# Optimization experiments

Hardware: AMD Instinct MI355X
Metric: run time of the kernel (lower is better)

## Reference

```python
import jax, jax.numpy as jnp
import numpy as np

HIDDEN = 256

def setup_inputs() -> dict:
    key = jax.random.key(0)
    k1, k2, k3, k4 = jax.random.split(key, 4)
    B, S, H = 64, 4096, HIDDEN
    o_all_time = jax.random.normal(k1, (B, S, H), dtype=jnp.float32)
    scale = 1.0 / np.sqrt(H)
    W_t = jax.random.uniform(k2, (H, H), dtype=jnp.float32, minval=-scale, maxval=scale)
    W_F = jax.random.uniform(k3, (H, H), dtype=jnp.float32, minval=-scale, maxval=scale)
    v_F = jax.random.uniform(k4, (H, 1), dtype=jnp.float32, minval=-scale, maxval=scale)
    return {"o_all_time": o_all_time, "W_t": W_t, "W_F": W_F, "v_F": v_F}

def reference(o_all_time, W_t, W_F, v_F):
    # o_all_time: (B, S, H)
    o_last = o_all_time[:, -1, :]                       # (B, H)
    # time attention: scores = o_last @ (o_all_time @ W_t)^T over seq
    M_t = jnp.einsum('bsh,hk->bsk', o_all_time, W_t)    # (B, S, H)
    scores_time = jnp.einsum('bh,bsh->bs', o_last, M_t) # (B, S)
    alpha_t = jax.nn.softmax(scores_time, axis=-1)      # (B, S)
    output_T = jnp.einsum('bs,bsh->bh', alpha_t, o_all_time)  # (B, H)
    # feature attention: softmax over seq of v_F^T tanh(W_F x)
    M_f = jnp.tanh(jnp.einsum('bsh,hk->bsk', o_all_time, W_F))  # (B, S, H)
    scores_feature = jnp.einsum('bsh,hk->bsk', M_f, v_F)[..., 0]  # (B, S)
    alpha_f = jax.nn.softmax(scores_feature, axis=1)    # (B, S)
    output_F = jnp.einsum('bs,bsh->bh', alpha_f, o_all_time)  # (B, H)
    return jnp.concatenate([output_T, output_F], axis=1)  # (B, 2H)
```

## Files before the change

kernel.cpp:

```cpp
#include <hip/hip_runtime.h>
#include <hip/hip_bf16.h>
#include <stdint.h>

#define HID 256
#define BATCH 64
#define SEQ 4096

typedef __attribute__((ext_vector_type(8))) short bf16x8;
typedef __attribute__((ext_vector_type(4))) short short4v;
typedef __attribute__((ext_vector_type(4))) float f32x4;

static __device__ __forceinline__ unsigned short f2bf(float f) {
    union { float f; uint32_t u; } v; v.f = f;
    uint32_t u = v.u;
    return (unsigned short)((u + 0x7FFF + ((u >> 16) & 1)) >> 16);
}

static __device__ __forceinline__ float fast_tanh(float x) {
    float cx = fminf(fmaxf(x, -15.f), 15.f);
    float e = __expf(2.f * cx);
    return (e - 1.f) / (e + 1.f);
}

__global__ __launch_bounds__(256) void prep_wft(const float* __restrict__ WF,
                                                unsigned short* __restrict__ WFt) {
    int c = blockIdx.x, h = threadIdx.x;
    WFt[c * HID + h] = f2bf(WF[h * HID + c]);
}

__global__ __launch_bounds__(256) void prep_ut(const float* __restrict__ o,
                                               const float* __restrict__ Wt,
                                               float* __restrict__ ut) {
    __shared__ float ol[HID];
    int b = blockIdx.x, h = threadIdx.x;
    ol[h] = o[(size_t)(b * SEQ + SEQ - 1) * HID + h];
    __syncthreads();
    const float* wrow = Wt + h * HID;
    float acc = 0.f;
    #pragma unroll 8
    for (int k = 0; k < HID; k++) acc += wrow[k] * ol[k];
    ut[b * HID + h] = acc;
}

__global__ __launch_bounds__(256, 4) void scores_kernel(const float* __restrict__ o,
                                                        const unsigned short* __restrict__ WFt,
                                                        const float* __restrict__ ut,
                                                        const float* __restrict__ vF,
                                                        float* __restrict__ stOut,
                                                        float* __restrict__ sfOut) {
    __shared__ unsigned short o_sm[64 * HID];
    __shared__ float u_sm[HID];
    __shared__ float red_sm[64 * 4];
    __shared__ float sfr[4 * 64];

    int t = threadIdx.x;
    int lane = t & 63, w = t >> 6;
    int bid = blockIdx.x;
    int b = bid >> 6;
    int s0 = (bid & 63) << 6;
    int lm = lane & 15, lg = lane >> 4;

    u_sm[t] = ut[b * HID + t];
    __syncthreads();

    const float* pbase = o + (size_t)(b * SEQ + s0) * HID + t * 4;
    const float4 u4 = *(const float4*)&u_sm[lane << 2];

    float4 va[8], vb[8];
    #pragma unroll
    for (int j = 0; j < 8; j++) va[j] = *(const float4*)(pbase + j * 1024);
    #pragma unroll
    for (int j = 0; j < 8; j++) vb[j] = *(const float4*)(pbase + (j + 8) * 1024);

    #pragma unroll
    for (int j = 0; j < 16; j++) {
        float4 v = (j < 8) ? va[j & 7] : vb[j & 7];
        int row = j * 4 + w;
        float p = v.x * u4.x + v.y * u4.y + v.z * u4.z + v.w * u4.w;
        p += __shfl_xor(p, 1);
        p += __shfl_xor(p, 2);
        p += __shfl_xor(p, 4);
        p += __shfl_xor(p, 8);
        if (lm == 0) red_sm[(row << 2) + lg] = p;
        int byte = (row << 9) + (lane << 3);
        byte ^= (row & 7) << 4;
        short4v sv;
        sv.x = (short)f2bf(v.x); sv.y = (short)f2bf(v.y);
        sv.z = (short)f2bf(v.z); sv.w = (short)f2bf(v.w);
        *(short4v*)((char*)o_sm + byte) = sv;
    }
    __syncthreads();

    if (t < 64) {
        const float* r4 = &red_sm[t << 2];
        stOut[(size_t)b * SEQ + s0 + t] = r4[0] + r4[1] + r4[2] + r4[3];
    }

    f32x4 acc[4][4];
    #pragma unroll
    for (int ar = 0; ar < 4; ar++)
        #pragma unroll
        for (int cb = 0; cb < 4; cb++)
            acc[ar][cb] = (f32x4){0.f, 0.f, 0.f, 0.f};

    int cw = w << 6;

    #pragma unroll
    for (int kk = 0; kk < 8; kk++) {
        int h0 = kk * 32 + lg * 8;
        bf16x8 bf[4], af[4];
        #pragma unroll
        for (int cb = 0; cb < 4; cb++) {
            int c = cw + cb * 16 + lm;
            bf[cb] = *(const bf16x8*)(WFt + (size_t)c * HID + h0);
        }
        #pragma unroll
        for (int ar = 0; ar < 4; ar++) {
            int row = ar * 16 + lm;
            int byte = (row << 9) + h0 * 2;
            byte ^= (row & 7) << 4;
            af[ar] = *(const bf16x8*)((const char*)o_sm + byte);
        }
        #pragma unroll
        for (int ar = 0; ar < 4; ar++)
            #pragma unroll
            for (int cb = 0; cb < 4; cb++)
                acc[ar][cb] = __builtin_amdgcn_mfma_f32_16x16x32_bf16(af[ar], bf[cb], acc[ar][cb], 0, 0, 0);
    }

    float vf[4];
    #pragma unroll
    for (int cb = 0; cb < 4; cb++) vf[cb] = vF[cw + cb * 16 + lm];

    #pragma unroll
    for (int ar = 0; ar < 4; ar++) {
        #pragma unroll
        for (int i = 0; i < 4; i++) {
            float p = 0.f;
            #pragma unroll
            for (int cb = 0; cb < 4; cb++)
                p += fast_tanh(acc[ar][cb][i]) * vf[cb];
            p += __shfl_xor(p, 1);
            p += __shfl_xor(p, 2);
            p += __shfl_xor(p, 4);
            p += __shfl_xor(p, 8);
            if (lm == 0) sfr[w * 64 + ar * 16 + lg * 4 + i] = p;
        }
    }
    __syncthreads();
    if (t < 64) {
        float s = sfr[t] + sfr[64 + t] + sfr[128 + t] + sfr[192 + t];
        sfOut[(size_t)b * SEQ + s0 + t] = s;
    }
}

template <bool MAXOP>
static __device__ __forceinline__ float block_reduce(float v, float* sh) {
    #pragma unroll
    for (int m = 1; m < 64; m <<= 1) {
        float o = __shfl_xor(v, m);
        v = MAXOP ? fmaxf(v, o) : (v + o);
    }
    int w = threadIdx.x >> 6;
    if ((threadIdx.x & 63) == 0) sh[w] = v;
    __syncthreads();
    float r = MAXOP ? fmaxf(fmaxf(sh[0], sh[1]), fmaxf(sh[2], sh[3]))
                    : (sh[0] + sh[1] + sh[2] + sh[3]);
    __syncthreads();
    return r;
}

__global__ __launch_bounds__(256) void stats_kernel(const float* __restrict__ st,
                                                    const float* __restrict__ sf,
                                                    float* __restrict__ stats) {
    __shared__ float sh[4];
    int b = blockIdx.x, t = threadIdx.x;
    const float* pt = st + (size_t)b * SEQ;
    const float* pf = sf + (size_t)b * SEQ;
    float vt[16], vf[16], mT = -1e30f, mF = -1e30f;
    #pragma unroll
    for (int j = 0; j < 16; j++) {
        vt[j] = pt[t + j * 256]; mT = fmaxf(mT, vt[j]);
        vf[j] = pf[t + j * 256]; mF = fmaxf(mF, vf[j]);
    }
    mT = block_reduce<true>(mT, sh);
    mF = block_reduce<true>(mF, sh);
    float sT = 0.f, sF = 0.f;
    #pragma unroll
    for (int j = 0; j < 16; j++) {
        sT += __expf(vt[j] - mT);
        sF += __expf(vf[j] - mF);
    }
    sT = block_reduce<false>(sT, sh);
    sF = block_reduce<false>(sF, sh);
    if (t == 0) {
        stats[b * 4 + 0] = mT;
        stats[b * 4 + 1] = sT;
        stats[b * 4 + 2] = mF;
        stats[b * 4 + 3] = sF;
    }
}

__global__ __launch_bounds__(256, 4) void out_kernel(const float* __restrict__ o,
                                                     const float* __restrict__ st,
                                                     const float* __restrict__ sf,
                                                     const float* __restrict__ stats,
                                                     float* __restrict__ out) {
    __shared__ float wT[128], wF[128];
    __shared__ float4 redT[4][64], redF[4][64];
    int bid = blockIdx.x;
    int b = bid >> 5, chunk = bid & 31, s0 = chunk << 7;
    int t = threadIdx.x;

    if (t < 128) {
        float mT = stats[b * 4 + 0], isT = 1.f / stats[b * 4 + 1];
        float mF = stats[b * 4 + 2], isF = 1.f / stats[b * 4 + 3];
        wT[t] = __expf(st[(size_t)b * SEQ + s0 + t] - mT) * isT;
        wF[t] = __expf(sf[(size_t)b * SEQ + s0 + t] - mF) * isF;
    }
    __syncthreads();

    int hc = t & 63, sl = t >> 6;
    const float* ob = o + (size_t)(b * SEQ + s0) * HID + hc * 4;
    float4 aT = {0.f, 0.f, 0.f, 0.f}, aF = {0.f, 0.f, 0.f, 0.f};
    #pragma unroll
    for (int ii = 0; ii < 4; ii++) {
        float4 v[8];
        #pragma unroll
        for (int k = 0; k < 8; k++) {
            int r = sl + (ii * 8 + k) * 4;
            v[k] = *(const float4*)(ob + (size_t)r * HID);
        }
        #pragma unroll
        for (int k = 0; k < 8; k++) {
            int r = sl + (ii * 8 + k) * 4;
            float wt = wT[r], wf = wF[r];
            aT.x += wt * v[k].x; aT.y += wt * v[k].y; aT.z += wt * v[k].z; aT.w += wt * v[k].w;
            aF.x += wf * v[k].x; aF.y += wf * v[k].y; aF.z += wf * v[k].z; aF.w += wf * v[k].w;
        }
    }
    redT[sl][hc] = aT;
    redF[sl][hc] = aF;
    __syncthreads();

    int hcc = t >> 2, i = t & 3;
    float sumT = 0.f, sumF = 0.f;
    #pragma unroll
    for (int p = 0; p < 4; p++) {
        sumT += ((const float*)&redT[p][hcc])[i];
        sumF += ((const float*)&redF[p][hcc])[i];
    }
    atomicAdd(out + (size_t)b * 512 + t, sumT);
    atomicAdd(out + (size_t)b * 512 + 256 + t, sumF);
}

extern "C" void kernel_launch(void* const* d_in, const int* in_sizes, int n_in,
                              void* d_out, int out_size, void* d_ws, size_t ws_size,
                              hipStream_t stream) {
    const float* o  = (const float*)d_in[0];
    const float* Wt = (const float*)d_in[1];
    const float* WF = (const float*)d_in[2];
    const float* vF = (const float*)d_in[3];
    float* out = (float*)d_out;
    char* ws = (char*)d_ws;

    unsigned short* WFt = (unsigned short*)ws;
    float* ut    = (float*)(ws + 131072);
    float* stS   = (float*)(ws + 196608);
    float* sfS   = (float*)(ws + 196608 + 1048576);
    float* stats = (float*)(ws + 196608 + 2097152);

    hipMemsetAsync(d_out, 0, (size_t)BATCH * 512 * sizeof(float), stream);
    prep_wft<<<256, 256, 0, stream>>>(WF, WFt);
    prep_ut<<<BATCH, 256, 0, stream>>>(o, Wt, ut);
    scores_kernel<<<BATCH * 64, 256, 0, stream>>>(o, WFt, ut, vF, stS, sfS);
    stats_kernel<<<BATCH, 256, 0, stream>>>(stS, sfS, stats);
    out_kernel<<<BATCH * 32, 256, 0, stream>>>(o, stS, sfS, stats, out);
}
```

Before: 460.8 us.

## Fuse score, local softmax and weighted sum into one pass with combine

Computes per-tile softmax statistics and weighted partial sums inside the scores kernel using the bf16 tile already staged in shared memory. A small combine kernel then merges the partials with log-sum-exp rescaling. This removes the second full read of o, the stats kernel, the memset and the atomics, and merges the two prep kernels into one launch. In exchange, the weighted sums now use bf16-rounded inputs, which lowers accuracy.

```diff
diff --git a/kernel.cpp b/kernel.cpp
--- a/kernel.cpp
+++ b/kernel.cpp
@@ -16,42 +16,54 @@
     return (unsigned short)((u + 0x7FFF + ((u >> 16) & 1)) >> 16);
 }
 
+static __device__ __forceinline__ float bf2f(unsigned short b) {
+    union { uint32_t u; float f; } v; v.u = ((uint32_t)b) << 16;
+    return v.f;
+}
+
 static __device__ __forceinline__ float fast_tanh(float x) {
     float cx = fminf(fmaxf(x, -15.f), 15.f);
     float e = __expf(2.f * cx);
     return (e - 1.f) / (e + 1.f);
 }
 
-__global__ __launch_bounds__(256) void prep_wft(const float* __restrict__ WF,
-                                                unsigned short* __restrict__ WFt) {
-    int c = blockIdx.x, h = threadIdx.x;
-    WFt[c * HID + h] = f2bf(WF[h * HID + c]);
-}
-
-__global__ __launch_bounds__(256) void prep_ut(const float* __restrict__ o,
-                                               const float* __restrict__ Wt,
-                                               float* __restrict__ ut) {
+__global__ __launch_bounds__(256) void prep_kernel(const float* __restrict__ WF,
+                                                   const float* __restrict__ Wt,
+                                                   const float* __restrict__ o,
+                                                   unsigned short* __restrict__ WFt,
+                                                   float* __restrict__ ut) {
     __shared__ float ol[HID];
-    int b = blockIdx.x, h = threadIdx.x;
-    ol[h] = o[(size_t)(b * SEQ + SEQ - 1) * HID + h];
-    __syncthreads();
-    const float* wrow = Wt + h * HID;
-    float acc = 0.f;
-    #pragma unroll 8
-    for (int k = 0; k < HID; k++) acc += wrow[k] * ol[k];
-    ut[b * HID + h] = acc;
-}
-
-__global__ __launch_bounds__(256, 4) void scores_kernel(const float* __restrict__ o,
-                                                        const unsigned short* __restrict__ WFt,
-                                                        const float* __restrict__ ut,
-                                                        const float* __restrict__ vF,
-                                                        float* __restrict__ stOut,
-                                                        float* __restrict__ sfOut) {
-    __shared__ unsigned short o_sm[64 * HID];
+    int bid = blockIdx.x, t = threadIdx.x;
+    if (bid < 256) {
+        WFt[bid * HID + t] = f2bf(WF[t * HID + bid]);
+    } else {
+        int b = bid - 256;
+        ol[t] = o[(size_t)(b * SEQ + SEQ - 1) * HID + t];
+        __syncthreads();
+        const float* wrow = Wt + t * HID;
+        float acc = 0.f;
+        #pragma unroll 16
+        for (int k = 0; k < HID; k += 4) {
+            float4 w4 = *(const float4*)(wrow + k);
+            float4 o4 = *(const float4*)(ol + k);
+            acc += w4.x * o4.x + w4.y * o4.y + w4.z * o4.z + w4.w * o4.w;
+        }
+        ut[b * HID + t] = acc;
+    }
+}
+
+__global__ __launch_bounds__(256, 4) void fused_kernel(const float* __restrict__ o,
+                                                       const unsigned short* __restrict__ WFt,
+                                                       const float* __restrict__ ut,
+                                                       const float* __restrict__ vF,
+                                                       float* __restrict__ pT,
+                                                       float* __restrict__ pF,
+                                                       float* __restrict__ stats4) {
+    __shared__ __align__(16) unsigned short o_sm[64 * HID];
     __shared__ float u_sm[HID];
-    __shared__ float red_sm[64 * 4];
-    __shared__ float sfr[4 * 64];
+    __shared__ float red_sm[256];
+    __shared__ float sfr[256];
+    __shared__ float st_sm[64], sf_sm[64], wT_sm[64], wF_sm[64];
 
     int t = threadIdx.x;
     int lane = t & 63, w = t >> 6;
@@ -93,7 +105,7 @@
 
     if (t < 64) {
         const float* r4 = &red_sm[t << 2];
-        stOut[(size_t)b * SEQ + s0 + t] = r4[0] + r4[1] + r4[2] + r4[3];
+        st_sm[t] = r4[0] + r4[1] + r4[2] + r4[3];
     }
 
     f32x4 acc[4][4];
@@ -104,7 +116,6 @@
             acc[ar][cb] = (f32x4){0.f, 0.f, 0.f, 0.f};
 
     int cw = w << 6;
-
     #pragma unroll
     for (int kk = 0; kk < 8; kk++) {
         int h0 = kk * 32 + lg * 8;
@@ -148,110 +159,112 @@
         }
     }
     __syncthreads();
-    if (t < 64) {
-        float s = sfr[t] + sfr[64 + t] + sfr[128 + t] + sfr[192 + t];
-        sfOut[(size_t)b * SEQ + s0 + t] = s;
-    }
-}
-
-template <bool MAXOP>
-static __device__ __forceinline__ float block_reduce(float v, float* sh) {
-    #pragma unroll
-    for (int m = 1; m < 64; m <<= 1) {
-        float o = __shfl_xor(v, m);
-        v = MAXOP ? fmaxf(v, o) : (v + o);
-    }
-    int w = threadIdx.x >> 6;
-    if ((threadIdx.x & 63) == 0) sh[w] = v;
-    __syncthreads();
-    float r = MAXOP ? fmaxf(fmaxf(sh[0], sh[1]), fmaxf(sh[2], sh[3]))
-                    : (sh[0] + sh[1] + sh[2] + sh[3]);
-    __syncthreads();
-    return r;
-}
-
-__global__ __launch_bounds__(256) void stats_kernel(const float* __restrict__ st,
-                                                    const float* __restrict__ sf,
-                                                    float* __restrict__ stats) {
-    __shared__ float sh[4];
+    if (t < 64) sf_sm[t] = sfr[t] + sfr[64 + t] + sfr[128 + t] + sfr[192 + t];
+    __syncthreads();
+
+    if (t < 64) {
+        float vT = st_sm[t], vfv = sf_sm[t];
+        float mT = vT, mF = vfv;
+        #pragma unroll
+        for (int d = 1; d < 64; d <<= 1) {
+            mT = fmaxf(mT, __shfl_xor(mT, d));
+            mF = fmaxf(mF, __shfl_xor(mF, d));
+        }
+        float wT = __expf(vT - mT), wF = __expf(vfv - mF);
+        wT_sm[t] = wT; wF_sm[t] = wF;
+        float lT = wT, lF = wF;
+        #pragma unroll
+        for (int d = 1; d < 64; d <<= 1) {
+            lT += __shfl_xor(lT, d);
+            lF += __shfl_xor(lF, d);
+        }
+        if (t == 0) {
+            float* s4 = stats4 + (size_t)bid * 4;
+            s4[0] = mT; s4[1] = lT; s4[2] = mF; s4[3] = lF;
+        }
+    }
+    __syncthreads();
+
+    float4 aT = {0.f, 0.f, 0.f, 0.f}, aF = {0.f, 0.f, 0.f, 0.f};
+    #pragma unroll
+    for (int j = 0; j < 16; j++) {
+        int row = j * 4 + w;
+        int byte = (row << 9) + (lane << 3);
+        byte ^= (row & 7) << 4;
+        short4v sv = *(const short4v*)((const char*)o_sm + byte);
+        float x0 = bf2f((unsigned short)sv.x), x1 = bf2f((unsigned short)sv.y);
+        float x2 = bf2f((unsigned short)sv.z), x3 = bf2f((unsigned short)sv.w);
+        float wt = wT_sm[row], wf = wF_sm[row];
+        aT.x += wt * x0; aT.y += wt * x1; aT.z += wt * x2; aT.w += wt * x3;
+        aF.x += wf * x0; aF.y += wf * x1; aF.z += wf * x2; aF.w += wf * x3;
+    }
+    __syncthreads();
+    float4* pTa = (float4*)&o_sm[0];
+    float4* pFa = (float4*)&o_sm[2048];
+    pTa[w * 64 + lane] = aT;
+    pFa[w * 64 + lane] = aF;
+    __syncthreads();
+
+    if (t < 64) {
+        float4 s = pTa[t];
+        #pragma unroll
+        for (int ww = 1; ww < 4; ww++) {
+            float4 q = pTa[ww * 64 + t];
+            s.x += q.x; s.y += q.y; s.z += q.z; s.w += q.w;
+        }
+        *(float4*)(pT + (size_t)bid * HID + (t << 2)) = s;
+    } else if (t < 128) {
+        int tt = t - 64;
+        float4 s = pFa[tt];
+        #pragma unroll
+        for (int ww = 1; ww < 4; ww++) {
+            float4 q = pFa[ww * 64 + tt];
+            s.x += q.x; s.y += q.y; s.z += q.z; s.w += q.w;
+        }
+        *(float4*)(pF + (size_t)bid * HID + (tt << 2)) = s;
+    }
+}
+
+__global__ __launch_bounds__(256) void combine_kernel(const float* __restrict__ pT,
+                                                      const float* __restrict__ pF,
+                                                      const float* __restrict__ stats4,
+                                                      float* __restrict__ out) {
+    __shared__ float sMT[64], sLT[64], sMF[64], sLF[64], eT[64], eF[64];
+    __shared__ float sc[2];
     int b = blockIdx.x, t = threadIdx.x;
-    const float* pt = st + (size_t)b * SEQ;
-    const float* pf = sf + (size_t)b * SEQ;
-    float vt[16], vf[16], mT = -1e30f, mF = -1e30f;
-    #pragma unroll
-    for (int j = 0; j < 16; j++) {
-        vt[j] = pt[t + j * 256]; mT = fmaxf(mT, vt[j]);
-        vf[j] = pf[t + j * 256]; mF = fmaxf(mF, vf[j]);
-    }
-    mT = block_reduce<true>(mT, sh);
-    mF = block_reduce<true>(mF, sh);
-    float sT = 0.f, sF = 0.f;
-    #pragma unroll
-    for (int j = 0; j < 16; j++) {
-        sT += __expf(vt[j] - mT);
-        sF += __expf(vf[j] - mF);
-    }
-    sT = block_reduce<false>(sT, sh);
-    sF = block_reduce<false>(sF, sh);
-    if (t == 0) {
-        stats[b * 4 + 0] = mT;
-        stats[b * 4 + 1] = sT;
-        stats[b * 4 + 2] = mF;
-        stats[b * 4 + 3] = sF;
-    }
-}
-
-__global__ __launch_bounds__(256, 4) void out_kernel(const float* __restrict__ o,
-                                                     const float* __restrict__ st,
-                                                     const float* __restrict__ sf,
-                                                     const float* __restrict__ stats,
-                                                     float* __restrict__ out) {
-    __shared__ float wT[128], wF[128];
-    __shared__ float4 redT[4][64], redF[4][64];
-    int bid = blockIdx.x;
-    int b = bid >> 5, chunk = bid & 31, s0 = chunk << 7;
-    int t = threadIdx.x;
-
-    if (t < 128) {
-        float mT = stats[b * 4 + 0], isT = 1.f / stats[b * 4 + 1];
-        float mF = stats[b * 4 + 2], isF = 1.f / stats[b * 4 + 3];
-        wT[t] = __expf(st[(size_t)b * SEQ + s0 + t] - mT) * isT;
-        wF[t] = __expf(sf[(size_t)b * SEQ + s0 + t] - mF) * isF;
-    }
-    __syncthreads();
-
-    int hc = t & 63, sl = t >> 6;
-    const float* ob = o + (size_t)(b * SEQ + s0) * HID + hc * 4;
-    float4 aT = {0.f, 0.f, 0.f, 0.f}, aF = {0.f, 0.f, 0.f, 0.f};
-    #pragma unroll
-    for (int ii = 0; ii < 4; ii++) {
-        float4 v[8];
-        #pragma unroll
-        for (int k = 0; k < 8; k++) {
-            int r = sl + (ii * 8 + k) * 4;
-            v[k] = *(const float4*)(ob + (size_t)r * HID);
-        }
-        #pragma unroll
-        for (int k = 0; k < 8; k++) {
-            int r = sl + (ii * 8 + k) * 4;
-            float wt = wT[r], wf = wF[r];
-            aT.x += wt * v[k].x; aT.y += wt * v[k].y; aT.z += wt * v[k].z; aT.w += wt * v[k].w;
-            aF.x += wf * v[k].x; aF.y += wf * v[k].y; aF.z += wf * v[k].z; aF.w += wf * v[k].w;
-        }
-    }
-    redT[sl][hc] = aT;
-    redF[sl][hc] = aF;
-    __syncthreads();
-
-    int hcc = t >> 2, i = t & 3;
-    float sumT = 0.f, sumF = 0.f;
-    #pragma unroll
-    for (int p = 0; p < 4; p++) {
-        sumT += ((const float*)&redT[p][hcc])[i];
-        sumF += ((const float*)&redF[p][hcc])[i];
-    }
-    atomicAdd(out + (size_t)b * 512 + t, sumT);
-    atomicAdd(out + (size_t)b * 512 + 256 + t, sumF);
+    if (t < 64) {
+        const float* s4 = stats4 + (size_t)(b * 64 + t) * 4;
+        sMT[t] = s4[0]; sLT[t] = s4[1]; sMF[t] = s4[2]; sLF[t] = s4[3];
+    }
+    __syncthreads();
+    if (t < 64) {
+        float mT = sMT[t], mF = sMF[t];
+        #pragma unroll
+        for (int d = 1; d < 64; d <<= 1) {
+            mT = fmaxf(mT, __shfl_xor(mT, d));
+            mF = fmaxf(mF, __shfl_xor(mF, d));
+        }
+        float wT = __expf(sMT[t] - mT), wF = __expf(sMF[t] - mF);
+        eT[t] = wT; eF[t] = wF;
+        float lT = wT * sLT[t], lF = wF * sLF[t];
+        #pragma unroll
+        for (int d = 1; d < 64; d <<= 1) {
+            lT += __shfl_xor(lT, d);
+            lF += __shfl_xor(lF, d);
+        }
+        if (t == 0) { sc[0] = lT; sc[1] = lF; }
+    }
+    __syncthreads();
+    float accT = 0.f, accF = 0.f;
+    const float* pTb = pT + (size_t)b * 64 * HID + t;
+    const float* pFb = pF + (size_t)b * 64 * HID + t;
+    #pragma unroll 8
+    for (int c = 0; c < 64; c++) {
+        accT += eT[c] * pTb[(size_t)c * HID];
+        accF += eF[c] * pFb[(size_t)c * HID];
+    }
+    out[b * 512 + t] = accT / sc[0];
+    out[b * 512 + 256 + t] = accF / sc[1];
 }
 
 extern "C" void kernel_launch(void* const* d_in, const int* in_sizes, int n_in,
@@ -265,15 +278,12 @@
     char* ws = (char*)d_ws;
 
     unsigned short* WFt = (unsigned short*)ws;
-    float* ut    = (float*)(ws + 131072);
-    float* stS   = (float*)(ws + 196608);
-    float* sfS   = (float*)(ws + 196608 + 1048576);
-    float* stats = (float*)(ws + 196608 + 2097152);
-
-    hipMemsetAsync(d_out, 0, (size_t)BATCH * 512 * sizeof(float), stream);
-    prep_wft<<<256, 256, 0, stream>>>(WF, WFt);
-    prep_ut<<<BATCH, 256, 0, stream>>>(o, Wt, ut);
-    scores_kernel<<<BATCH * 64, 256, 0, stream>>>(o, WFt, ut, vF, stS, sfS);
-    stats_kernel<<<BATCH, 256, 0, stream>>>(stS, sfS, stats);
-    out_kernel<<<BATCH * 32, 256, 0, stream>>>(o, stS, sfS, stats, out);
-}
+    float* ut     = (float*)(ws + 131072);
+    float* pT     = (float*)(ws + 196608);
+    float* pF     = (float*)(ws + 196608 + 4194304);
+    float* stats4 = (float*)(ws + 196608 + 8388608);
+
+    prep_kernel<<<320, 256, 0, stream>>>(WF, Wt, o, WFt, ut);
+    fused_kernel<<<BATCH * 64, 256, 0, stream>>>(o, WFt, ut, vF, pT, pF, stats4);
+    combine_kernel<<<BATCH, 256, 0, stream>>>(pT, pF, stats4, out);
+}
```

After: 452.3 us. About the same (-1.8%).
